# Performance work log

Hardware: AMD Instinct MI355X
Metric: run time of the kernel (lower is better)

## Reference

```python
import jax, jax.numpy as jnp
import numpy as np

# DeHoog ILT constants (from init_kwargs)
ALPHA = 1e-3
TOL = 1e-2          # default tol = 10*alpha
SCALE = 2.0
NTERMS = 33         # ilt_reconstruction_terms = 2M+1
M = (NTERMS - 1) // 2


def setup_inputs() -> dict:
    key = jax.random.key(0)
    k1, k2, k3 = jax.random.split(key, 3)
    B, S, D = 32, 512, 32
    # positive, sorted time points; T = ti (recommended usage)
    ti = jnp.sort(jax.random.uniform(k1, (S,), minval=0.5, maxval=1.5))
    T = ti
    Tsc = SCALE * T                                     # contour period per time point
    gamma = ALPHA - jnp.log(TOL) / (SCALE * Tsc)        # (S,)
    kk = jnp.arange(NTERMS)
    s = gamma[:, None] + 1j * jnp.pi * kk[None, :] / Tsc[:, None]   # (S, 33)
    # Build fp as a genuine Laplace transform F(s) = sum_p c_p / (s + w_p)
    # (random fp makes the QD recurrence numerically singular)
    P = 4
    w = jax.random.uniform(k2, (B, D, P), minval=0.2, maxval=3.0)
    c = jax.random.normal(k3, (B, D, P))
    fp = jnp.zeros((B, S, D, NTERMS), dtype=jnp.complex64)
    for p in range(P):  # small fixed loop over poles, avoids a (B,S,D,P,33) intermediate
        fp = fp + c[:, None, :, p, None] / (s[None, :, None, :] + w[:, None, :, p, None])
    return {
        "fp_real": jnp.real(fp).astype(jnp.float32),
        "fp_imag": jnp.imag(fp).astype(jnp.float32),
        "ti": ti.astype(jnp.float32),
        "T": T.astype(jnp.float32),
    }


def _dehoog(fp_real, fp_imag, ti, T):
    """De Hoog ILT: QD (quotient-difference) Pade acceleration + continued
    fraction with remainder term. fp: (B,S,D,2M+1) complex samples of F at
    s_{i,k} = gamma_i + i*pi*k/T_i.  Returns x(t): (B,S,D) real."""
    fp = fp_real + 1j * fp_imag                       # (B,S,D,2M+1)
    Tsc = SCALE * T                                   # (S,)
    gamma = ALPHA - jnp.log(TOL) / (SCALE * Tsc)      # (S,)
    # Fourier coefficients: a_0 halved
    a = jnp.concatenate([0.5 * fp[..., :1], fp[..., 1:]], axis=-1)
    # --- QD algorithm: builds continued-fraction coefficients d_0..d_{2M} ---
    q = a[..., 1:] / a[..., :-1]                      # q_1, length 2M
    e = jnp.zeros_like(a)                             # e_0 = 0, length 2M+1
    d = [a[..., 0], -q[..., 0]]                       # d_0, d_1
    for r in range(1, M + 1):
        Le = 2 * (M - r) + 1
        e = q[..., 1:Le + 1] - q[..., :Le] + e[..., 1:Le + 1]   # e_r
        d.append(-e[..., 0])                          # d_{2r}
        if r < M:
            Lq = 2 * (M - r)
            q = q[..., 1:Lq + 1] * e[..., 1:Lq + 1] / e[..., :Lq]  # q_{r+1}
            d.insert(-1, -q[..., 0])                  # d_{2r+1} goes before d_{2r}? no-op below
    # fix ordering: rebuild d in canonical order [d0, -q1, -e1, -q2, -e2, ...]
    # (the insert above is wrong ordering; recompute cleanly)
    q = a[..., 1:] / a[..., :-1]
    e = jnp.zeros_like(a)
    d = [a[..., 0], -q[..., 0]]
    for r in range(1, M + 1):
        Le = 2 * (M - r) + 1
        e = q[..., 1:Le + 1] - q[..., :Le] + e[..., 1:Le + 1]
        if r < M:
            Lq = 2 * (M - r)
            q = q[..., 1:Lq + 1] * e[..., 1:Lq + 1] / e[..., :Lq]
            d.append(-e[..., 0])   # d_{2r}
            d.append(-q[..., 0])   # d_{2r+1}
        else:
            d.append(-e[..., 0])   # d_{2M}
    d = jnp.stack(d, axis=-1)                         # (B,S,D,2M+1)
    # --- continued fraction A_n = A_{n-1} + d_n z A_{n-2} via scan ---
    z = jnp.exp(1j * jnp.pi * (ti / Tsc))[None, :, None]   # (1,S,1)
    dz = jnp.moveaxis(d[..., 1:], -1, 0) * z          # (2M,B,S,D)
    A_prev = jnp.zeros_like(d[..., 0])
    A_cur = d[..., 0]
    B_prev = jnp.ones_like(A_cur)
    B_cur = jnp.ones_like(A_cur)
    def step(carry, dzn):
        Ap, Ac, Bp, Bc = carry
        return (Ac, Ac + dzn * Ap, Bc, Bc + dzn * Bp), None
    (A_prev, A_cur, B_prev, B_cur), _ = jax.lax.scan(step, (A_prev, A_cur, B_prev, B_cur), dz)
    # --- double acceleration: remainder term for the truncated fraction ---
    brem = 0.5 * (1.0 + (d[..., 2 * M - 1] - d[..., 2 * M]) * z)
    rem = -brem * (1.0 - jnp.sqrt(1.0 + d[..., 2 * M] * z / (brem * brem)))
    Af = A_cur + rem * A_prev
    Bf = B_cur + rem * B_prev
    return (jnp.exp(gamma * ti) / Tsc)[None, :, None] * jnp.real(Af / Bf)


def reference(fp_real, fp_imag, ti, T):
    return _dehoog(fp_real, fp_imag, ti, T)
```

## Files before the change

### kernel.cpp

```cpp
#include <hip/hip_runtime.h>
#include <math.h>

#define MM 8
#define NU (2*MM + 1)
#define NT 33
#define DD 32
#define SS 512
#define BLK 64
#define ROWS_PER_BLK 128
#define CHUNK_ROWS 64
#define CHUNK_FLOATS (CHUNK_ROWS * NT)

typedef float f2 __attribute__((ext_vector_type(2)));

struct c2 { f2 re, im; };

__device__ __forceinline__ f2 mkf2(float a, float b) { f2 v; v.x = a; v.y = b; return v; }

__device__ __forceinline__ f2 rcp2(f2 d) {
    f2 r;
    r.x = __builtin_amdgcn_rcpf(d.x);
    r.y = __builtin_amdgcn_rcpf(d.y);
    return r * (2.0f - d * r);
}
__device__ __forceinline__ f2 sqrt2f(f2 x) { f2 r; r.x = sqrtf(x.x); r.y = sqrtf(x.y); return r; }

__device__ __forceinline__ c2 cmul(c2 a, c2 b) {
    c2 o;
    o.re = a.re * b.re - a.im * b.im;
    o.im = a.re * b.im + a.im * b.re;
    return o;
}
__device__ __forceinline__ c2 cadd(c2 a, c2 b) { c2 o; o.re = a.re + b.re; o.im = a.im + b.im; return o; }
__device__ __forceinline__ c2 csub(c2 a, c2 b) { c2 o; o.re = a.re - b.re; o.im = a.im - b.im; return o; }
__device__ __forceinline__ c2 cneg(c2 a) { c2 o; o.re = -a.re; o.im = -a.im; return o; }
__device__ __forceinline__ c2 cdiv(c2 a, c2 b) {
    f2 d = b.re * b.re + b.im * b.im;
    d = __builtin_elementwise_max(d, mkf2(1.0e-32f, 1.0e-32f));
    f2 r = rcp2(d);
    c2 o;
    o.re = (a.re * b.re + a.im * b.im) * r;
    o.im = (a.im * b.re - a.re * b.im) * r;
    return o;
}
__device__ __forceinline__ c2 csqrt2(c2 a) {
    f2 r = sqrt2f(a.re * a.re + a.im * a.im);
    f2 re = sqrt2f(__builtin_elementwise_max(0.5f * (r + a.re), mkf2(0.0f, 0.0f)));
    f2 im = sqrt2f(__builtin_elementwise_max(0.5f * (r - a.re), mkf2(0.0f, 0.0f)));
    im.x = (a.im.x < 0.0f) ? -im.x : im.x;
    im.y = (a.im.y < 0.0f) ? -im.y : im.y;
    c2 o; o.re = re; o.im = im; return o;
}

__device__ __forceinline__ void gload_lds16(const float* gp, float* lp) {
    __builtin_amdgcn_global_load_lds(
        (const __attribute__((address_space(1))) void*)gp,
        (__attribute__((address_space(3))) void*)lp,
        16, 0, 0);
}

__global__ __launch_bounds__(BLK, 4) void dehoog_kernel(
    const float* __restrict__ fpr, const float* __restrict__ fpi,
    const float* __restrict__ ti_arr, const float* __restrict__ T_arr,
    float* __restrict__ out)
{
    __shared__ float lbuf[CHUNK_FLOATS];

    const int l = threadIdx.x;
    const int b = blockIdx.x;

    const size_t blk_base = (size_t)b * ROWS_PER_BLK * NT;
    const float* gR = fpr + blk_base;
    const float* gI = fpi + blk_base;

    auto stage = [&](const float* g, int chunk) {
        const float* gc = g + chunk * CHUNK_FLOATS;
#pragma unroll
        for (int k = 0; k < 8; ++k)
            gload_lds16(gc + (size_t)(k * 64 + l) * 4, lbuf + k * 256);
        if (l < 16)
            gload_lds16(gc + (size_t)(512 + l) * 4, lbuf + 2048);
    };

    f2 ar[NU], ai[NU];

    stage(gR, 0);
    __syncthreads();
    {
        const float* row = lbuf + l * NT;
#pragma unroll
        for (int j = 0; j < NU; ++j) ar[j].x = row[j];
    }
    __syncthreads();
    stage(gR, 1);
    __syncthreads();
    {
        const float* row = lbuf + l * NT;
#pragma unroll
        for (int j = 0; j < NU; ++j) ar[j].y = row[j];
    }
    __syncthreads();
    stage(gI, 0);
    __syncthreads();
    {
        const float* row = lbuf + l * NT;
#pragma unroll
        for (int j = 0; j < NU; ++j) ai[j].x = row[j];
    }
    __syncthreads();
    stage(gI, 1);
    __syncthreads();
    {
        const float* row = lbuf + l * NT;
#pragma unroll
        for (int j = 0; j < NU; ++j) ai[j].y = row[j];
    }

    const int eA = b * ROWS_PER_BLK + l;
    const int eB = eA + 64;
    const int sA = (eA / DD) % SS;
    const int sB = (eB / DD) % SS;
    const f2 Tt  = mkf2(T_arr[sA],  T_arr[sB]);
    const f2 tii = mkf2(ti_arr[sA], ti_arr[sB]);
    const f2 Tsc = 2.0f * Tt;
    const f2 rTsc = rcp2(Tsc);
    const f2 gamma = 1.0e-3f + 4.605170185988091f * 0.5f * rTsc;

    c2 zc;
    {
        f2 ang = 3.14159265358979323846f * tii * rTsc;
        zc.re = mkf2(__cosf(ang.x), __cosf(ang.y));
        zc.im = mkf2(__sinf(ang.x), __sinf(ang.y));
    }

    c2 q[2 * MM];
    c2 e[NU];
    c2 a_prev; a_prev.re = 0.5f * ar[0]; a_prev.im = 0.5f * ai[0];
    const c2 d0 = a_prev;
#pragma unroll
    for (int j = 0; j < 2 * MM; ++j) {
        c2 a_next; a_next.re = ar[j + 1]; a_next.im = ai[j + 1];
        q[j] = cdiv(a_next, a_prev);
        a_prev = a_next;
    }
#pragma unroll
    for (int j = 0; j < NU; ++j) { e[j].re = mkf2(0.0f, 0.0f); e[j].im = mkf2(0.0f, 0.0f); }

    c2 Ap; Ap.re = mkf2(0.0f, 0.0f); Ap.im = mkf2(0.0f, 0.0f);
    c2 Ac = d0;
    c2 Bp; Bp.re = mkf2(1.0f, 1.0f); Bp.im = mkf2(0.0f, 0.0f);
    c2 Bc = Bp;

    auto cf_step = [&](c2 dn) {
        c2 dz = cmul(dn, zc);
        c2 An = cadd(Ac, cmul(dz, Ap));
        Ap = Ac; Ac = An;
        c2 Bn = cadd(Bc, cmul(dz, Bp));
        Bp = Bc; Bc = Bn;
    };

    c2 d_2M_m1; d_2M_m1.re = mkf2(0.0f, 0.0f); d_2M_m1.im = mkf2(0.0f, 0.0f);
    c2 d_2M;    d_2M.re    = mkf2(0.0f, 0.0f); d_2M.im    = mkf2(0.0f, 0.0f);

    cf_step(cneg(q[0]));

#pragma unroll
    for (int r = 1; r <= MM; ++r) {
        const int Le = 2 * (MM - r) + 1;
#pragma unroll
        for (int j = 0; j < Le; ++j)
            e[j] = cadd(csub(q[j + 1], q[j]), e[j + 1]);
        c2 d2r = cneg(e[0]);
        if (r < MM) {
            cf_step(d2r);
            const int Lq = 2 * (MM - r);
#pragma unroll
            for (int j = 0; j < Lq; ++j)
                q[j] = cdiv(cmul(q[j + 1], e[j + 1]), e[j]);
            c2 d2r1 = cneg(q[0]);
            cf_step(d2r1);
            if (r == MM - 1) d_2M_m1 = d2r1;
        } else {
            d_2M = d2r;
            cf_step(d2r);
        }
    }

    c2 ddv = csub(d_2M_m1, d_2M);
    c2 brem;
    {
        c2 t = cmul(ddv, zc);
        brem.re = 0.5f * (1.0f + t.re);
        brem.im = 0.5f * t.im;
    }
    c2 b2 = cmul(brem, brem);
    c2 arg = cdiv(cmul(d_2M, zc), b2);
    arg.re = 1.0f + arg.re;
    c2 sq = csqrt2(arg);
    c2 one_m; one_m.re = 1.0f - sq.re; one_m.im = -sq.im;
    c2 rem = cmul(cneg(brem), one_m);

    c2 Af = cadd(Ac, cmul(rem, Ap));
    c2 Bf = cadd(Bc, cmul(rem, Bp));

    f2 rden = rcp2(Bf.re * Bf.re + Bf.im * Bf.im);
    f2 re = (Af.re * Bf.re + Af.im * Bf.im) * rden;
    f2 expg; expg.x = __expf(gamma.x * tii.x); expg.y = __expf(gamma.y * tii.y);
    f2 res = expg * rTsc * re;

    out[eA] = res.x;
    out[eB] = res.y;
}

extern "C" void kernel_launch(void* const* d_in, const int* in_sizes, int n_in,
                              void* d_out, int out_size, void* d_ws, size_t ws_size,
                              hipStream_t stream) {
    const float* fpr = (const float*)d_in[0];
    const float* fpi = (const float*)d_in[1];
    const float* ti  = (const float*)d_in[2];
    const float* T   = (const float*)d_in[3];
    float* out = (float*)d_out;
    const int total = out_size;
    const int grid  = total / ROWS_PER_BLK;
    dehoog_kernel<<<grid, BLK, 0, stream>>>(fpr, fpi, ti, T, out);
}
```

Before: 166.1 us.

## Use 256-thread blocks with per-wave LDS staging and waitcnt instead of barriers

Blocks grow from one wave to four, and each wave gets a private LDS region, so staging needs no block-wide __syncthreads. Explicit vmcnt/lgkmcnt waits with sched barriers replace the barriers. The first QD iteration is peeled so the e array needs no zero-initialisation, which trims some register traffic. The risk is that the inline waitcnt and sched barriers constrain the scheduler, and the larger LDS footprint per block may lower occupancy.

```diff
diff --git a/kernel.cpp b/kernel.cpp
--- a/kernel.cpp
+++ b/kernel.cpp
@@ -6,10 +6,8 @@
 #define NT 33
 #define DD 32
 #define SS 512
-#define BLK 64
-#define ROWS_PER_BLK 128
-#define CHUNK_ROWS 64
-#define CHUNK_FLOATS (CHUNK_ROWS * NT)
+#define BLK 256
+#define CHUNK_FLOATS (64 * NT)
 
 typedef float f2 __attribute__((ext_vector_type(2)));
 
@@ -59,65 +57,66 @@
         16, 0, 0);
 }
 
-__global__ __launch_bounds__(BLK, 4) void dehoog_kernel(
+#define WAIT_VM()   do { asm volatile("s_waitcnt vmcnt(0)" ::: "memory"); \
+                         __builtin_amdgcn_sched_barrier(0); } while (0)
+#define WAIT_LGKM() do { asm volatile("s_waitcnt lgkmcnt(0)" ::: "memory"); \
+                         __builtin_amdgcn_sched_barrier(0); } while (0)
+
+__global__ void __launch_bounds__(BLK)
+__attribute__((amdgpu_waves_per_eu(4, 4)))
+dehoog_kernel(
     const float* __restrict__ fpr, const float* __restrict__ fpi,
     const float* __restrict__ ti_arr, const float* __restrict__ T_arr,
     float* __restrict__ out)
 {
-    __shared__ float lbuf[CHUNK_FLOATS];
-
-    const int l = threadIdx.x;
-    const int b = blockIdx.x;
-
-    const size_t blk_base = (size_t)b * ROWS_PER_BLK * NT;
-    const float* gR = fpr + blk_base;
-    const float* gI = fpi + blk_base;
-
-    auto stage = [&](const float* g, int chunk) {
-        const float* gc = g + chunk * CHUNK_FLOATS;
+    __shared__ float sbuf[4 * CHUNK_FLOATS];
+
+    const int t = threadIdx.x;
+    const int l = t & 63;
+    const int w = t >> 6;
+    float* lbuf = sbuf + w * CHUNK_FLOATS;
+
+    const int rowbase = blockIdx.x * 512 + w * 128;
+    const int eA = rowbase + l;
+    const int eB = eA + 64;
+
+    const float* gR = fpr + (size_t)rowbase * NT;
+    const float* gI = fpi + (size_t)rowbase * NT;
+
+    auto stage = [&](const float* g) {
 #pragma unroll
         for (int k = 0; k < 8; ++k)
-            gload_lds16(gc + (size_t)(k * 64 + l) * 4, lbuf + k * 256);
+            gload_lds16(g + (size_t)(k * 64 + l) * 4, lbuf + k * 256);
         if (l < 16)
-            gload_lds16(gc + (size_t)(512 + l) * 4, lbuf + 2048);
+            gload_lds16(g + (size_t)(512 + l) * 4, lbuf + 2048);
     };
 
-    f2 ar[NU], ai[NU];
-
-    stage(gR, 0);
-    __syncthreads();
-    {
-        const float* row = lbuf + l * NT;
-#pragma unroll
-        for (int j = 0; j < NU; ++j) ar[j].x = row[j];
-    }
-    __syncthreads();
-    stage(gR, 1);
-    __syncthreads();
-    {
-        const float* row = lbuf + l * NT;
-#pragma unroll
-        for (int j = 0; j < NU; ++j) ar[j].y = row[j];
-    }
-    __syncthreads();
-    stage(gI, 0);
-    __syncthreads();
-    {
-        const float* row = lbuf + l * NT;
-#pragma unroll
-        for (int j = 0; j < NU; ++j) ai[j].x = row[j];
-    }
-    __syncthreads();
-    stage(gI, 1);
-    __syncthreads();
-    {
-        const float* row = lbuf + l * NT;
-#pragma unroll
-        for (int j = 0; j < NU; ++j) ai[j].y = row[j];
-    }
-
-    const int eA = b * ROWS_PER_BLK + l;
-    const int eB = eA + 64;
+    c2 a_[NU];
+
+    stage(gR);
+    WAIT_VM();
+    { const float* row = lbuf + l * NT;
+#pragma unroll
+      for (int j = 0; j < NU; ++j) a_[j].re.x = row[j]; }
+    WAIT_LGKM();
+    stage(gR + 64 * NT);
+    WAIT_VM();
+    { const float* row = lbuf + l * NT;
+#pragma unroll
+      for (int j = 0; j < NU; ++j) a_[j].re.y = row[j]; }
+    WAIT_LGKM();
+    stage(gI);
+    WAIT_VM();
+    { const float* row = lbuf + l * NT;
+#pragma unroll
+      for (int j = 0; j < NU; ++j) a_[j].im.x = row[j]; }
+    WAIT_LGKM();
+    stage(gI + 64 * NT);
+    WAIT_VM();
+    { const float* row = lbuf + l * NT;
+#pragma unroll
+      for (int j = 0; j < NU; ++j) a_[j].im.y = row[j]; }
+
     const int sA = (eA / DD) % SS;
     const int sB = (eB / DD) % SS;
     const f2 Tt  = mkf2(T_arr[sA],  T_arr[sB]);
@@ -134,17 +133,14 @@
     }
 
     c2 q[2 * MM];
-    c2 e[NU];
-    c2 a_prev; a_prev.re = 0.5f * ar[0]; a_prev.im = 0.5f * ai[0];
+    c2 a_prev; a_prev.re = 0.5f * a_[0].re; a_prev.im = 0.5f * a_[0].im;
     const c2 d0 = a_prev;
 #pragma unroll
     for (int j = 0; j < 2 * MM; ++j) {
-        c2 a_next; a_next.re = ar[j + 1]; a_next.im = ai[j + 1];
+        c2 a_next = a_[j + 1];
         q[j] = cdiv(a_next, a_prev);
         a_prev = a_next;
     }
-#pragma unroll
-    for (int j = 0; j < NU; ++j) { e[j].re = mkf2(0.0f, 0.0f); e[j].im = mkf2(0.0f, 0.0f); }
 
     c2 Ap; Ap.re = mkf2(0.0f, 0.0f); Ap.im = mkf2(0.0f, 0.0f);
     c2 Ac = d0;
@@ -164,8 +160,17 @@
 
     cf_step(cneg(q[0]));
 
-#pragma unroll
-    for (int r = 1; r <= MM; ++r) {
+    c2 e[2 * MM - 1];
+#pragma unroll
+    for (int j = 0; j < 15; ++j) e[j] = csub(q[j + 1], q[j]);
+    cf_step(cneg(e[0]));
+#pragma unroll
+    for (int j = 0; j < 14; ++j)
+        q[j] = cdiv(cmul(q[j + 1], e[j + 1]), e[j]);
+    cf_step(cneg(q[0]));
+
+#pragma unroll
+    for (int r = 2; r <= MM; ++r) {
         const int Le = 2 * (MM - r) + 1;
 #pragma unroll
         for (int j = 0; j < Le; ++j)
@@ -189,9 +194,9 @@
     c2 ddv = csub(d_2M_m1, d_2M);
     c2 brem;
     {
-        c2 t = cmul(ddv, zc);
-        brem.re = 0.5f * (1.0f + t.re);
-        brem.im = 0.5f * t.im;
+        c2 tt = cmul(ddv, zc);
+        brem.re = 0.5f * (1.0f + tt.re);
+        brem.im = 0.5f * tt.im;
     }
     c2 b2 = cmul(brem, brem);
     c2 arg = cdiv(cmul(d_2M, zc), b2);
@@ -221,6 +226,6 @@
     const float* T   = (const float*)d_in[3];
     float* out = (float*)d_out;
     const int total = out_size;
-    const int grid  = total / ROWS_PER_BLK;
+    const int grid  = total / 512;
     dehoog_kernel<<<grid, BLK, 0, stream>>>(fpr, fpi, ti, T, out);
 }
```

After: 173.4 us. 4.4% more time.
